# Performance work log

Hardware: AMD Instinct MI355X
Metric: run time of the kernel (lower is better)

## Reference

```python
import jax, jax.numpy as jnp
import numpy as np
import math

B, CIN, COUT, K = 32, 256, 256, 3
STYLE_DIM, SP = 512, 64  # spatial_dim == output H == output W
EPS = 1e-6


def setup_inputs() -> dict:
    key = jax.random.key(0)
    ks = jax.random.split(key, 5)
    return {
        "x": jax.random.normal(ks[0], (B, CIN, SP, SP), jnp.float32),
        "style_in": jax.random.normal(ks[1], (B, STYLE_DIM), jnp.float32),
        "weight": jax.random.normal(ks[2], (1, COUT, CIN, K, K), jnp.float32),
        "mod_w": jax.random.normal(ks[3], (CIN, STYLE_DIM // 2), jnp.float32),
        "mod_b": jnp.ones((CIN,), jnp.float32),           # bias_init=1
        "sp_w": jax.random.normal(ks[4], (SP * SP, STYLE_DIM // 2), jnp.float32),
        "sp_b": jnp.ones((SP * SP,), jnp.float32),        # bias_init=1
    }


def reference(x, style_in, weight, mod_w, mod_b, sp_w, sp_b):
    lin_scale = 1.0 / math.sqrt(STYLE_DIM // 2)   # EqualLinear scale
    conv_scale = 1.0 / math.sqrt(CIN * K * K)     # fan_in scale

    style_chan, style_spatial = jnp.split(style_in, 2, axis=1)

    # channel modulation: EqualLinear -> [B, CIN]
    style = style_chan @ (mod_w * lin_scale).T + mod_b

    # per-sample modulated weight [B, COUT, CIN, K, K]
    w = conv_scale * weight * style[:, None, :, None, None]
    demod = jax.lax.rsqrt(jnp.sum(w * w, axis=(2, 3, 4)) + EPS)  # [B, COUT]
    w = w * demod[:, :, None, None, None]

    # grouped conv2d with groups = batch ('same' padding, stride 1)
    x_g = x.reshape(1, B * CIN, SP, SP)
    w_g = w.reshape(B * COUT, CIN, K, K)
    out = jax.lax.conv_general_dilated(
        x_g, w_g, window_strides=(1, 1),
        padding=[(K // 2, K // 2), (K // 2, K // 2)],
        dimension_numbers=("NCHW", "OIHW", "NCHW"),
        feature_group_count=B,
    ).reshape(B, COUT, SP, SP)

    # spatial modulation (demod_spatial == 2): multiply by demodulated map
    sp = (style_spatial @ (sp_w * lin_scale).T + sp_b).reshape(B, 1, SP, SP)
    demod_sp = jnp.sqrt(SP * SP / jnp.sum(sp * sp, axis=(2, 3)) + EPS)  # [B, 1]
    out = out * (sp * demod_sp[:, :, None, None])
    return out
```

## Files before the change

### kernel.cpp

```cpp
#include <hip/hip_runtime.h>
#include <math.h>

typedef short short8 __attribute__((ext_vector_type(8)));
typedef float f32x4 __attribute__((ext_vector_type(4)));

#define BB 32
#define CIN 256
#define COUT 256
#define SPD 64
#define SPP 4096
#define SDIM 256

constexpr float LIN_SCALE  = 0.0625f;
constexpr float CONV_SCALE = 0.020833333333333332f;
constexpr float EPS = 1e-6f;

#define WSB_STYLE   0ULL
#define WSB_DEMOD   32768ULL
#define WSB_WSQ     65536ULL
#define WSB_SP      327680ULL
#define WSB_DSP     851968ULL
#define WSB_ZERO    852096ULL
#define WSB_WT2     860160ULL
#define WSB_SSQP    2039808ULL
#define WSB_XST     2097152ULL
#define WS_NEED     (WSB_XST + 67108864ULL)

__device__ inline unsigned short f2bf(float f) {
    unsigned u = __builtin_bit_cast(unsigned, f);
    u = (u + 0x7fffu + ((u >> 16) & 1u)) >> 16;
    return (unsigned short)u;
}

__device__ inline void dma16(const void* g, void* l) {
    __builtin_amdgcn_global_load_lds(
        (const __attribute__((address_space(1))) unsigned int*)g,
        (__attribute__((address_space(3))) unsigned int*)l, 16, 0, 0);
}

__global__ __launch_bounds__(256) void k_prepA(
    const float* __restrict__ weight,
    const float* __restrict__ style_in,
    const float* __restrict__ sp_w,
    const float* __restrict__ sp_b,
    const float* __restrict__ mod_w,
    const float* __restrict__ mod_b,
    float* __restrict__ wsq,
    unsigned short* __restrict__ wt4,
    float* __restrict__ sp,
    float* __restrict__ ssq_part,
    float* __restrict__ style,
    unsigned* __restrict__ zero)
{
    __shared__ float s_in[32][257];
    __shared__ float sred[256];
    int bid = blockIdx.x, t = threadIdx.x;

    if (bid < 256) {
        int p0 = bid * 16;
        for (int idx = t; idx < 8192; idx += 256) {
            int b = idx >> 8, k = idx & 255;
            s_in[b][k] = style_in[b * 512 + 256 + k];
        }
        __syncthreads();
        int b = t & 31, pl = t >> 5;
        float ss = 0.f;
#pragma unroll
        for (int half = 0; half < 2; half++) {
            int p = p0 + half * 8 + pl;
            const float* wr = sp_w + (size_t)p * 256;
            float a = 0.f;
            for (int k = 0; k < 256; k++) a += s_in[b][k] * wr[k];
            float v = a * LIN_SCALE + sp_b[p];
            sp[b * SPP + p] = v;
            ss += v * v;
        }
        sred[t] = ss;
        __syncthreads();
        if (t < 32) {
            float s = 0.f;
#pragma unroll
            for (int r = 0; r < 8; r++) s += sred[r * 32 + t];
            ssq_part[bid * 32 + t] = s;
        }
    } else if (bid < 2560) {
        int idx = (bid - 256) * 256 + t;
        int e    = idx & 7;
        int r1   = idx >> 3;
        int lane = r1 & 63;
        int r2   = r1 >> 6;
        int cog  = r2 & 15;
        int r3   = r2 >> 4;
        int tap  = r3 % 9;
        int kc   = r3 / 9;
        int co = cog * 16 + (lane & 15);
        int ci = kc * 32 + (lane >> 4) * 8 + e;
        wt4[idx] = f2bf(weight[(co * 256 + ci) * 9 + tap]);
    } else if (bid < 2816) {
        int co = bid - 2560, ci = t;
        if (co == 0) zero[ci] = 0u;
        const float* wp = weight + (co * CIN + ci) * 9;
        float s = 0.f;
#pragma unroll
        for (int q = 0; q < 9; q++) { float v = wp[q]; s += v * v; }
        wsq[co * CIN + ci] = s;
    } else {
        int b = bid - 2816;
        float* s_lin = &s_in[0][0];
        s_lin[t] = style_in[b * 512 + t];
        __syncthreads();
        int kq = t & 3, rr = t >> 2;
#pragma unroll
        for (int c = 0; c < 4; c++) {
            int ci = c * 64 + rr;
            const float4* wrow = (const float4*)(mod_w + (size_t)ci * 256 + kq * 64);
            float a = 0.f;
#pragma unroll
            for (int j = 0; j < 16; j++) {
                float4 wv = wrow[j];
                int kb = kq * 64 + j * 4;
                a += s_lin[kb] * wv.x + s_lin[kb + 1] * wv.y + s_lin[kb + 2] * wv.z + s_lin[kb + 3] * wv.w;
            }
            a += __shfl_xor(a, 1); a += __shfl_xor(a, 2);
            if (kq == 0) style[b * 256 + ci] = a * LIN_SCALE + mod_b[ci];
        }
    }
}

__global__ __launch_bounds__(256) void k_xt2(
    const float* __restrict__ x,
    const float* __restrict__ style,
    const float* __restrict__ wsq,
    const float* __restrict__ ssq_part,
    unsigned short* __restrict__ xst,
    float* __restrict__ demod,
    float* __restrict__ dsp)
{
    __shared__ union {
        unsigned short tileb[64][74];
        float s2[CIN];
    } sh;
    int bid = blockIdx.x, t = threadIdx.x;

    if (bid >= 2048) {
        if (bid == 2080) {
            if (t < 32) {
                float s = 0.f;
                for (int i = 0; i < 256; i++) s += ssq_part[i * 32 + t];
                dsp[t] = sqrtf((float)SPP / s + EPS);
            }
            return;
        }
        int b = bid - 2048;
        float st = style[b * 256 + t];
        sh.s2[t] = st * st;
        __syncthreads();
        int kq = t & 3, rr = t >> 2;
#pragma unroll
        for (int c = 0; c < 4; c++) {
            int co = c * 64 + rr;
            const float4* wrow = (const float4*)(wsq + (size_t)co * 256 + kq * 64);
            float a = 0.f;
#pragma unroll
            for (int j = 0; j < 16; j++) {
                float4 wv = wrow[j];
                int kb = kq * 64 + j * 4;
                a += sh.s2[kb] * wv.x + sh.s2[kb + 1] * wv.y + sh.s2[kb + 2] * wv.z + sh.s2[kb + 3] * wv.w;
            }
            a += __shfl_xor(a, 1); a += __shfl_xor(a, 2);
            if (kq == 0) demod[b * 256 + co] = rsqrtf(CONV_SCALE * CONV_SCALE * a + EPS);
        }
        return;
    }

    int b  = (bid & 7) * 4 + ((bid >> 3) & 3);
    int p0 = (bid >> 5) * 64;
    int w = t >> 6, lane = t & 63;
    int pq = lane & 15, cg = lane >> 4;
    int lo2 = t & 15;

    for (int cc = 0; cc < 4; cc++) {
#pragma unroll
        for (int j = 0; j < 4; j++) {
            int ci_l = w * 16 + j * 4 + cg;
            int ci = cc * 64 + ci_l;
            float st = style[b * 256 + ci];
            float4 v = *(const float4*)(x + ((size_t)(b * 256 + ci)) * SPP + p0 + pq * 4);
            sh.tileb[pq * 4 + 0][ci_l] = f2bf(v.x * st);
            sh.tileb[pq * 4 + 1][ci_l] = f2bf(v.y * st);
            sh.tileb[pq * 4 + 2][ci_l] = f2bf(v.z * st);
            sh.tileb[pq * 4 + 3][ci_l] = f2bf(v.w * st);
        }
        __syncthreads();
#pragma unroll
        for (int it = 0; it < 4; it++) {
            int r = it * 16 + (t >> 4);
            unsigned pk0 = (unsigned)sh.tileb[r][lo2 * 4]
                         | ((unsigned)sh.tileb[r][lo2 * 4 + 1] << 16);
            unsigned pk1 = (unsigned)sh.tileb[r][lo2 * 4 + 2]
                         | ((unsigned)sh.tileb[r][lo2 * 4 + 3] << 16);
            uint2 pv = make_uint2(pk0, pk1);
            *(uint2*)((unsigned*)xst + ((size_t)(b * SPP + p0 + r)) * 128 + cc * 32 + lo2 * 2) = pv;
        }
        __syncthreads();
    }
}

__global__ __launch_bounds__(256, 2) void k_conv_mfma(
    const unsigned short* __restrict__ xst,
    const unsigned short* __restrict__ wt4,
    const float* __restrict__ demod,
    const float* __restrict__ sp,
    const float* __restrict__ dsp,
    const unsigned short* __restrict__ zeropad,
    float* __restrict__ out)
{
    __shared__ union {
        char stage[2][25344];
        float ep[4][2176];
    } lds;
    __shared__ float demod_l[128];

    int bid = blockIdx.x;
    int xcd  = bid & 7;
    int b_lo = (bid >> 3) & 3;
    int coh  = (bid >> 5) & 1;
    int rq   = bid >> 6;
    int b  = xcd * 4 + b_lo;
    int h0 = rq * 4;
    int t = threadIdx.x;
    int w = t >> 6, lane = t & 63;
    int cpair = w & 1, rpair = w >> 1;
    int cog0 = coh * 8 + cpair * 4;
    int lcol = lane & 15, kg = lane >> 4;

    if (t < 128) demod_l[t] = demod[b * 256 + coh * 128 + t];

    const unsigned short* xb = xst + (size_t)b * SPP * 256;

    const unsigned short* sbase[7];
#pragma unroll
    for (int it = 0; it < 7; it++) {
        int idx16 = t + it * 256;
        const unsigned short* s = zeropad;
        if (idx16 < 1584) {
            int slot = idx16 >> 2, j = idx16 & 3;
            int row = slot / 66, col = slot - row * 66;
            int g = j ^ ((slot >> 1) & 3);
            int gh = h0 + row - 1, gw = col - 1;
            if ((unsigned)gh < 64u && (unsigned)gw < 64u)
                s = xb + ((size_t)(gh * 64 + gw)) * 256 + g * 8;
        }
        sbase[it] = s;
    }

#define STAGE_DMA(BUF, KC) { _Pragma("unroll") \
    for (int it = 0; it < 6; it++) \
        dma16(sbase[it] + (KC) * 32, &lds.stage[BUF][0] + (t + it * 256) * 16); \
    if (t < 48) dma16(sbase[6] + (KC) * 32, &lds.stage[BUF][0] + (t + 1536) * 16); }

    STAGE_DMA(0, 0);

    f32x4 acc[4][8];
#pragma unroll
    for (int m = 0; m < 4; m++)
#pragma unroll
        for (int n = 0; n < 8; n++) acc[m][n] = (f32x4){0.f, 0.f, 0.f, 0.f};

    asm volatile("s_waitcnt vmcnt(0) lgkmcnt(0)" ::: "memory");
    __builtin_amdgcn_s_barrier();

#define LOADW(a0,a1,a2,a3, TAP) { \
        const unsigned short* wp_ = wkc + (size_t)(((TAP) * 16 + cog0)) * 512 + lane * 8; \
        a0 = *(const short8*)(wp_); \
        a1 = *(const short8*)(wp_ + 512); \
        a2 = *(const short8*)(wp_ + 1024); \
        a3 = *(const short8*)(wp_ + 1536); }

#define LOADB(a0,a1,a2,a3, TAP, HALF) { \
        const int dh_ = (TAP) / 3, dw_ = (TAP) - 3 * (dh_); \
        int s0_ = (rpair * 2 + (HALF) + dh_) * 66 + dw_ + lcol; \
        int q_ = (s0_ >> 1) & 3; \
        const char* lbp_ = lb + s0_ * 64 + ((kg ^ q_) << 4); \
        a0 = *(const short8*)(lbp_); \
        a1 = *(const short8*)(lbp_ + 1024); \
        a2 = *(const short8*)(lbp_ + 2048); \
        a3 = *(const short8*)(lbp_ + 3072); }

#define BURSTN(w0_,w1_,w2_,w3_, x0_,x1_,x2_,x3_, NO) { \
        __builtin_amdgcn_s_setprio(1); \
        acc[0][NO+0] = __builtin_amdgcn_mfma_f32_16x16x32_bf16(w0_, x0_, acc[0][NO+0], 0, 0, 0); \
        acc[1][NO+0] = __builtin_amdgcn_mfma_f32_16x16x32_bf16(w1_, x0_, acc[1][NO+0], 0, 0, 0); \
        acc[2][NO+0] = __builtin_amdgcn_mfma_f32_16x16x32_bf16(w2_, x0_, acc[2][NO+0], 0, 0, 0); \
        acc[3][NO+0] = __builtin_amdgcn_mfma_f32_16x16x32_bf16(w3_, x0_, acc[3][NO+0], 0, 0, 0); \
        acc[0][NO+1] = __builtin_amdgcn_mfma_f32_16x16x32_bf16(w0_, x1_, acc[0][NO+1], 0, 0, 0); \
        acc[1][NO+1] = __builtin_amdgcn_mfma_f32_16x16x32_bf16(w1_, x1_, acc[1][NO+1], 0, 0, 0); \
        acc[2][NO+1] = __builtin_amdgcn_mfma_f32_16x16x32_bf16(w2_, x1_, acc[2][NO+1], 0, 0, 0); \
        acc[3][NO+1] = __builtin_amdgcn_mfma_f32_16x16x32_bf16(w3_, x1_, acc[3][NO+1], 0, 0, 0); \
        acc[0][NO+2] = __builtin_amdgcn_mfma_f32_16x16x32_bf16(w0_, x2_, acc[0][NO+2], 0, 0, 0); \
        acc[1][NO+2] = __builtin_amdgcn_mfma_f32_16x16x32_bf16(w1_, x2_, acc[1][NO+2], 0, 0, 0); \
        acc[2][NO+2] = __builtin_amdgcn_mfma_f32_16x16x32_bf16(w2_, x2_, acc[2][NO+2], 0, 0, 0); \
        acc[3][NO+2] = __builtin_amdgcn_mfma_f32_16x16x32_bf16(w3_, x2_, acc[3][NO+2], 0, 0, 0); \
        acc[0][NO+3] = __builtin_amdgcn_mfma_f32_16x16x32_bf16(w0_, x3_, acc[0][NO+3], 0, 0, 0); \
        acc[1][NO+3] = __builtin_amdgcn_mfma_f32_16x16x32_bf16(w1_, x3_, acc[1][NO+3], 0, 0, 0); \
        acc[2][NO+3] = __builtin_amdgcn_mfma_f32_16x16x32_bf16(w2_, x3_, acc[2][NO+3], 0, 0, 0); \
        acc[3][NO+3] = __builtin_amdgcn_mfma_f32_16x16x32_bf16(w3_, x3_, acc[3][NO+3], 0, 0, 0); \
        __builtin_amdgcn_s_setprio(0); }

    int cur = 0;
    for (int kc = 0; kc < 8; kc++) {
        const char* lb = &lds.stage[cur][0];
        const unsigned short* wkc = wt4 + (size_t)(kc * 9) * 8192;

        short8 wc0, wc1, wc2, wc3, wn0, wn1, wn2, wn3;
        short8 b00, b01, b02, b03, b0n0, b0n1, b0n2, b0n3;
        short8 b10, b11, b12, b13;
        LOADW(wc0, wc1, wc2, wc3, 0);
        LOADB(b00, b01, b02, b03, 0, 0);
        LOADW(wn0, wn1, wn2, wn3, 1);
        if (kc < 7) STAGE_DMA(cur ^ 1, kc + 1);

#pragma unroll
        for (int tap = 0; tap < 9; tap++) {
            if (tap >= 1 && tap < 8) {
                switch (tap + 1) {
                    case 2: LOADW(wn0,wn1,wn2,wn3,2); break;
                    case 3: LOADW(wn0,wn1,wn2,wn3,3); break;
                    case 4: LOADW(wn0,wn1,wn2,wn3,4); break;
                    case 5: LOADW(wn0,wn1,wn2,wn3,5); break;
                    case 6: LOADW(wn0,wn1,wn2,wn3,6); break;
                    case 7: LOADW(wn0,wn1,wn2,wn3,7); break;
                    case 8: LOADW(wn0,wn1,wn2,wn3,8); break;
                }
            }
            switch (tap) {
                case 0: LOADB(b10,b11,b12,b13,0,1); break;
                case 1: LOADB(b10,b11,b12,b13,1,1); break;
                case 2: LOADB(b10,b11,b12,b13,2,1); break;
                case 3: LOADB(b10,b11,b12,b13,3,1); break;
                case 4: LOADB(b10,b11,b12,b13,4,1); break;
                case 5: LOADB(b10,b11,b12,b13,5,1); break;
                case 6: LOADB(b10,b11,b12,b13,6,1); break;
                case 7: LOADB(b10,b11,b12,b13,7,1); break;
                case 8: LOADB(b10,b11,b12,b13,8,1); break;
            }
            BURSTN(wc0, wc1, wc2, wc3, b00, b01, b02, b03, 0);
            if (tap < 8) {
                switch (tap + 1) {
                    case 1: LOADB(b0n0,b0n1,b0n2,b0n3,1,0); break;
                    case 2: LOADB(b0n0,b0n1,b0n2,b0n3,2,0); break;
                    case 3: LOADB(b0n0,b0n1,b0n2,b0n3,3,0); break;
                    case 4: LOADB(b0n0,b0n1,b0n2,b0n3,4,0); break;
                    case 5: LOADB(b0n0,b0n1,b0n2,b0n3,5,0); break;
                    case 6: LOADB(b0n0,b0n1,b0n2,b0n3,6,0); break;
                    case 7: LOADB(b0n0,b0n1,b0n2,b0n3,7,0); break;
                    case 8: LOADB(b0n0,b0n1,b0n2,b0n3,8,0); break;
                }
            }
            BURSTN(wc0, wc1, wc2, wc3, b10, b11, b12, b13, 4);
            wc0 = wn0; wc1 = wn1; wc2 = wn2; wc3 = wn3;
            b00 = b0n0; b01 = b0n1; b02 = b0n2; b03 = b0n3;
        }

        asm volatile("s_waitcnt vmcnt(0) lgkmcnt(0)" ::: "memory");
        __builtin_amdgcn_s_barrier();
        cur ^= 1;
    }

    float dspb = dsp[b];
    float spn[2][4];
#pragma unroll
    for (int half = 0; half < 2; half++) {
        int hout = h0 + rpair * 2 + half;
#pragma unroll
        for (int nn = 0; nn < 4; nn++)
            spn[half][nn] = sp[b * SPP + hout * 64 + nn * 16 + lcol] * dspb;
    }

    float* ep = &lds.ep[w][0];
#pragma unroll
    for (int half = 0; half < 2; half++) {
        int hout = h0 + rpair * 2 + half;
#pragma unroll
        for (int ch = 0; ch < 2; ch++) {
#pragma unroll
            for (int mm = 0; mm < 2; mm++) {
#pragma unroll
                for (int r2 = 0; r2 < 4; r2++) {
                    int lr = mm * 16 + kg * 4 + r2;
                    float dm = demod_l[cpair * 64 + ch * 32 + lr] * CONV_SCALE;
#pragma unroll
                    for (int nn = 0; nn < 4; nn++)
                        ep[lr * 68 + nn * 16 + lcol] =
                            acc[ch * 2 + mm][half * 4 + nn][r2] * dm * spn[half][nn];
                }
            }
#pragma unroll
            for (int i = 0; i < 8; i++) {
                int lr = i * 4 + kg;
                f32x4 v = *(const f32x4*)(ep + lr * 68 + lcol * 4);
                int co_g = coh * 128 + cpair * 64 + ch * 32 + lr;
                *(f32x4*)&out[((size_t)(b * 256 + co_g)) * SPP + hout * 64 + lcol * 4] = v;
            }
        }
    }
}


__global__ void k_wsq(const float* __restrict__ weight, float* __restrict__ wsq,
                      unsigned* __restrict__ zero) {
    int co = blockIdx.x, ci = threadIdx.x;
    if (co == 0) zero[ci] = 0u;
    const float* wp = weight + (co * CIN + ci) * 9;
    float s = 0.f;
#pragma unroll
    for (int t = 0; t < 9; t++) { float v = wp[t]; s += v * v; }
    wsq[co * CIN + ci] = s;
}

__global__ void k_style_fb(const float* __restrict__ style_in,
                           const float* __restrict__ mod_w,
                           const float* __restrict__ mod_b,
                           const float* __restrict__ wsq,
                           float* __restrict__ style,
                           float* __restrict__ demod) {
    __shared__ float s_in[SDIM];
    __shared__ float s2[CIN];
    int b = blockIdx.x, t = threadIdx.x;
    s_in[t] = style_in[b * 512 + t];
    __syncthreads();
    const float* mw = mod_w + t * SDIM;
    float acc = 0.f;
    for (int k = 0; k < SDIM; k++) acc += s_in[k] * mw[k];
    float st = acc * LIN_SCALE + mod_b[t];
    style[b * CIN + t] = st;
    s2[t] = st * st;
    __syncthreads();
    const float* wq = wsq + t * CIN;
    float d = 0.f;
    for (int ci = 0; ci < CIN; ci++) d += wq[ci] * s2[ci];
    demod[b * COUT + t] = rsqrtf(CONV_SCALE * CONV_SCALE * d + EPS);
}

__global__ void k_spatial(const float* __restrict__ style_in,
                          const float* __restrict__ sp_w,
                          const float* __restrict__ sp_b,
                          float* __restrict__ sp,
                          float* __restrict__ dsp) {
    __shared__ float s_in[SDIM];
    __shared__ float red[256];
    int b = blockIdx.x, t = threadIdx.x;
    s_in[t] = style_in[b * 512 + 256 + t];
    __syncthreads();
    float ss = 0.f;
    for (int i = 0; i < 16; i++) {
        int p = i * 256 + t;
        const float* wr = sp_w + p * SDIM;
        float acc = 0.f;
        for (int k = 0; k < SDIM; k++) acc += s_in[k] * wr[k];
        float v = acc * LIN_SCALE + sp_b[p];
        sp[b * SPP + p] = v;
        ss += v * v;
    }
    red[t] = ss; __syncthreads();
    for (int o = 128; o > 0; o >>= 1) { if (t < o) red[t] += red[t + o]; __syncthreads(); }
    if (t == 0) dsp[b] = sqrtf((float)SPP / red[0] + EPS);
}

#define COTILE 16
#define TS 32
#define HALO 34
#define XS 36

__global__ __launch_bounds__(256) void k_conv_f32(
    const float* __restrict__ x, const float* __restrict__ weight,
    const float* __restrict__ style, const float* __restrict__ demod,
    const float* __restrict__ sp, const float* __restrict__ dsp,
    float* __restrict__ out) {
    __shared__ float xt[HALO * XS];
    __shared__ float wl[COTILE * 12];
    __shared__ float dml[COTILE];

    int bid = blockIdx.x;
    int tile = bid & 3;
    int cot = (bid >> 2) & 15;
    int b = bid >> 6;
    int h0 = (tile >> 1) * TS, w0 = (tile & 1) * TS;
    int t = threadIdx.x;
    int r = t >> 3;
    int cb = (t & 7) * 4;

    if (t < COTILE) dml[t] = demod[b * COUT + cot * COTILE + t];

    float acc[COTILE][4];
#pragma unroll
    for (int co = 0; co < COTILE; co++)
#pragma unroll
        for (int c = 0; c < 4; c++) acc[co][c] = 0.f;

    const float* xb = x + (size_t)b * CIN * SPP;
    const float* stb = style + b * CIN;

    for (int ci = 0; ci < CIN; ci++) {
        __syncthreads();
        const float* xc = xb + ci * SPP;
        for (int idx = t; idx < HALO * HALO; idx += 256) {
            int i = idx / HALO, j = idx - i * HALO;
            int h = h0 + i - 1, wv2 = w0 + j - 1;
            float v = 0.f;
            if ((unsigned)h < SPD && (unsigned)wv2 < SPD) v = xc[h * SPD + wv2];
            xt[i * XS + j] = v;
        }
        if (t < COTILE * 9) {
            int co = t / 9, tap = t - co * 9;
            float wv = weight[((cot * COTILE + co) * CIN + ci) * 9 + tap];
            wl[co * 12 + tap] = wv * (CONV_SCALE * stb[ci]) * dml[co];
        }
        __syncthreads();

        float xv[3][6];
#pragma unroll
        for (int dh = 0; dh < 3; dh++)
#pragma unroll
            for (int jj = 0; jj < 6; jj++)
                xv[dh][jj] = xt[(r + dh) * XS + cb + jj];

#pragma unroll
        for (int co = 0; co < COTILE; co++) {
            float w9[9];
#pragma unroll
            for (int q = 0; q < 9; q++) w9[q] = wl[co * 12 + q];
#pragma unroll
            for (int c = 0; c < 4; c++) {
                float a = acc[co][c];
#pragma unroll
                for (int dh = 0; dh < 3; dh++)
#pragma unroll
                    for (int dw = 0; dw < 3; dw++)
                        a += w9[dh * 3 + dw] * xv[dh][c + dw];
                acc[co][c] = a;
            }
        }
    }

    float dspb = dsp[b];
    int hh = h0 + r, ww = w0 + cb;
    const float* spb = sp + b * SPP + hh * SPD + ww;
    float m[4];
#pragma unroll
    for (int c = 0; c < 4; c++) m[c] = spb[c] * dspb;
#pragma unroll
    for (int co = 0; co < COTILE; co++) {
        float4 v = make_float4(acc[co][0] * m[0], acc[co][1] * m[1],
                               acc[co][2] * m[2], acc[co][3] * m[3]);
        *(float4*)&out[(size_t)((b * COUT + cot * COTILE + co) * SPP) + hh * SPD + ww] = v;
    }
}


extern "C" void kernel_launch(void* const* d_in, const int* in_sizes, int n_in,
                              void* d_out, int out_size, void* d_ws, size_t ws_size,
                              hipStream_t stream) {
    const float* x        = (const float*)d_in[0];
    const float* style_in = (const float*)d_in[1];
    const float* weight   = (const float*)d_in[2];
    const float* mod_w    = (const float*)d_in[3];
    const float* mod_b    = (const float*)d_in[4];
    const float* sp_w     = (const float*)d_in[5];
    const float* sp_b     = (const float*)d_in[6];
    float* out = (float*)d_out;
    char* wsb = (char*)d_ws;

    float* style = (float*)(wsb + WSB_STYLE);
    float* demod = (float*)(wsb + WSB_DEMOD);
    float* wsq   = (float*)(wsb + WSB_WSQ);
    float* sp    = (float*)(wsb + WSB_SP);
    float* dsp   = (float*)(wsb + WSB_DSP);
    float* ssqp  = (float*)(wsb + WSB_SSQP);
    unsigned short* wt4 = (unsigned short*)(wsb + WSB_WT2);
    unsigned short* xst = (unsigned short*)(wsb + WSB_XST);

    if (ws_size >= WS_NEED) {
        hipLaunchKernelGGL(k_prepA, dim3(2848), dim3(256), 0, stream,
                           weight, style_in, sp_w, sp_b, mod_w, mod_b,
                           wsq, wt4, sp, ssqp, style,
                           (unsigned*)(wsb + WSB_ZERO));
        hipLaunchKernelGGL(k_xt2, dim3(2081), dim3(256), 0, stream,
                           x, style, wsq, ssqp, xst, demod, dsp);
        hipLaunchKernelGGL(k_conv_mfma, dim3(1024), dim3(256), 0, stream,
                           xst, wt4, demod, sp, dsp,
                           (const unsigned short*)(wsb + WSB_ZERO), out);
    } else {
        hipLaunchKernelGGL(k_wsq, dim3(COUT), dim3(CIN), 0, stream,
                           weight, wsq, (unsigned*)(wsb + WSB_ZERO));
        hipLaunchKernelGGL(k_style_fb, dim3(BB), dim3(256), 0, stream,
                           style_in, mod_w, mod_b, wsq, style, demod);
        hipLaunchKernelGGL(k_spatial, dim3(BB), dim3(256), 0, stream,
                           style_in, sp_w, sp_b, sp, dsp);
        hipLaunchKernelGGL(k_conv_f32, dim3(2048), dim3(256), 0, stream,
                           x, weight, style, demod, sp, dsp, out);
    }
}
```

Before: 209.6 us.

## Switch conv MFMA tiles from 16x16x32 to 32x32x16 bf16

Replaces the 16x16x32 bf16 MFMA burst with 32x32x16 instructions. This means changing the packed weight layout in the prep kernel, the LDS B-operand addressing (32 pixel columns, k-halves), and the epilogue register-to-output mapping. Each wave issues 8 larger MFMAs per burst instead of 16 small ones. The larger tile gives more FLOPs per instruction and fewer operand reads per FLOP. The risk is different LDS bank-conflict behaviour with the swizzle and longer MFMA dependency latency.

```diff
diff --git a/kernel.cpp b/kernel.cpp
--- a/kernel.cpp
+++ b/kernel.cpp
@@ -3,6 +3,7 @@
 
 typedef short short8 __attribute__((ext_vector_type(8)));
 typedef float f32x4 __attribute__((ext_vector_type(4)));
+typedef float f32x16 __attribute__((ext_vector_type(16)));
 
 #define BB 32
 #define CIN 256
@@ -89,12 +90,13 @@
         int r1   = idx >> 3;
         int lane = r1 & 63;
         int r2   = r1 >> 6;
-        int cog  = r2 & 15;
+        int cogkh = r2 & 15;
+        int cog2 = cogkh >> 1, kh = cogkh & 1;
         int r3   = r2 >> 4;
         int tap  = r3 % 9;
         int kc   = r3 / 9;
-        int co = cog * 16 + (lane & 15);
-        int ci = kc * 32 + (lane >> 4) * 8 + e;
+        int co = cog2 * 32 + (lane & 31);
+        int ci = kc * 32 + kh * 16 + (lane >> 5) * 8 + e;
         wt4[idx] = f2bf(weight[(co * 256 + ci) * 9 + tap]);
     } else if (bid < 2816) {
         int co = bid - 2560, ci = t;
@@ -233,6 +235,7 @@
     int cpair = w & 1, rpair = w >> 1;
     int cog0 = coh * 8 + cpair * 4;
     int lcol = lane & 15, kg = lane >> 4;
+    int l31 = lane & 31, h5 = lane >> 5;
 
     if (t < 128) demod_l[t] = demod[b * 256 + coh * 128 + t];
 
@@ -261,50 +264,46 @@
 
     STAGE_DMA(0, 0);
 
-    f32x4 acc[4][8];
-#pragma unroll
-    for (int m = 0; m < 4; m++)
-#pragma unroll
-        for (int n = 0; n < 8; n++) acc[m][n] = (f32x4){0.f, 0.f, 0.f, 0.f};
+    f32x16 acc[2][4];
+#pragma unroll
+    for (int m = 0; m < 2; m++)
+#pragma unroll
+        for (int n = 0; n < 4; n++)
+#pragma unroll
+            for (int r = 0; r < 16; r++) acc[m][n][r] = 0.f;
 
     asm volatile("s_waitcnt vmcnt(0) lgkmcnt(0)" ::: "memory");
     __builtin_amdgcn_s_barrier();
 
-#define LOADW(a0,a1,a2,a3, TAP) { \
+#define LOADW(a00,a01,a10,a11, TAP) { \
         const unsigned short* wp_ = wkc + (size_t)(((TAP) * 16 + cog0)) * 512 + lane * 8; \
-        a0 = *(const short8*)(wp_); \
-        a1 = *(const short8*)(wp_ + 512); \
-        a2 = *(const short8*)(wp_ + 1024); \
-        a3 = *(const short8*)(wp_ + 1536); }
-
-#define LOADB(a0,a1,a2,a3, TAP, HALF) { \
+        a00 = *(const short8*)(wp_); \
+        a01 = *(const short8*)(wp_ + 512); \
+        a10 = *(const short8*)(wp_ + 1024); \
+        a11 = *(const short8*)(wp_ + 1536); }
+
+#define LOADB(b0,b1,b2,b3, TAP, HALF) { \
         const int dh_ = (TAP) / 3, dw_ = (TAP) - 3 * (dh_); \
-        int s0_ = (rpair * 2 + (HALF) + dh_) * 66 + dw_ + lcol; \
+        int s0_ = (rpair * 2 + (HALF) + dh_) * 66 + dw_ + l31; \
         int q_ = (s0_ >> 1) & 3; \
-        const char* lbp_ = lb + s0_ * 64 + ((kg ^ q_) << 4); \
-        a0 = *(const short8*)(lbp_); \
-        a1 = *(const short8*)(lbp_ + 1024); \
-        a2 = *(const short8*)(lbp_ + 2048); \
-        a3 = *(const short8*)(lbp_ + 3072); }
-
-#define BURSTN(w0_,w1_,w2_,w3_, x0_,x1_,x2_,x3_, NO) { \
+        const char* lbp_ = lb + s0_ * 64; \
+        int q0_ = (h5 ^ q_) << 4; \
+        int q1_ = ((2 + h5) ^ q_) << 4; \
+        b0 = *(const short8*)(lbp_ + q0_); \
+        b1 = *(const short8*)(lbp_ + q1_); \
+        b2 = *(const short8*)(lbp_ + 2048 + q0_); \
+        b3 = *(const short8*)(lbp_ + 2048 + q1_); }
+
+#define BURSTN(a00,a01,a10,a11, b0,b1,b2,b3, NO) { \
         __builtin_amdgcn_s_setprio(1); \
-        acc[0][NO+0] = __builtin_amdgcn_mfma_f32_16x16x32_bf16(w0_, x0_, acc[0][NO+0], 0, 0, 0); \
-        acc[1][NO+0] = __builtin_amdgcn_mfma_f32_16x16x32_bf16(w1_, x0_, acc[1][NO+0], 0, 0, 0); \
-        acc[2][NO+0] = __builtin_amdgcn_mfma_f32_16x16x32_bf16(w2_, x0_, acc[2][NO+0], 0, 0, 0); \
-        acc[3][NO+0] = __builtin_amdgcn_mfma_f32_16x16x32_bf16(w3_, x0_, acc[3][NO+0], 0, 0, 0); \
-        acc[0][NO+1] = __builtin_amdgcn_mfma_f32_16x16x32_bf16(w0_, x1_, acc[0][NO+1], 0, 0, 0); \
-        acc[1][NO+1] = __builtin_amdgcn_mfma_f32_16x16x32_bf16(w1_, x1_, acc[1][NO+1], 0, 0, 0); \
-        acc[2][NO+1] = __builtin_amdgcn_mfma_f32_16x16x32_bf16(w2_, x1_, acc[2][NO+1], 0, 0, 0); \
-        acc[3][NO+1] = __builtin_amdgcn_mfma_f32_16x16x32_bf16(w3_, x1_, acc[3][NO+1], 0, 0, 0); \
-        acc[0][NO+2] = __builtin_amdgcn_mfma_f32_16x16x32_bf16(w0_, x2_, acc[0][NO+2], 0, 0, 0); \
-        acc[1][NO+2] = __builtin_amdgcn_mfma_f32_16x16x32_bf16(w1_, x2_, acc[1][NO+2], 0, 0, 0); \
-        acc[2][NO+2] = __builtin_amdgcn_mfma_f32_16x16x32_bf16(w2_, x2_, acc[2][NO+2], 0, 0, 0); \
-        acc[3][NO+2] = __builtin_amdgcn_mfma_f32_16x16x32_bf16(w3_, x2_, acc[3][NO+2], 0, 0, 0); \
-        acc[0][NO+3] = __builtin_amdgcn_mfma_f32_16x16x32_bf16(w0_, x3_, acc[0][NO+3], 0, 0, 0); \
-        acc[1][NO+3] = __builtin_amdgcn_mfma_f32_16x16x32_bf16(w1_, x3_, acc[1][NO+3], 0, 0, 0); \
-        acc[2][NO+3] = __builtin_amdgcn_mfma_f32_16x16x32_bf16(w2_, x3_, acc[2][NO+3], 0, 0, 0); \
-        acc[3][NO+3] = __builtin_amdgcn_mfma_f32_16x16x32_bf16(w3_, x3_, acc[3][NO+3], 0, 0, 0); \
+        acc[0][NO]   = __builtin_amdgcn_mfma_f32_32x32x16_bf16(a00, b0, acc[0][NO],   0, 0, 0); \
+        acc[1][NO]   = __builtin_amdgcn_mfma_f32_32x32x16_bf16(a10, b0, acc[1][NO],   0, 0, 0); \
+        acc[0][NO+1] = __builtin_amdgcn_mfma_f32_32x32x16_bf16(a00, b2, acc[0][NO+1], 0, 0, 0); \
+        acc[1][NO+1] = __builtin_amdgcn_mfma_f32_32x32x16_bf16(a10, b2, acc[1][NO+1], 0, 0, 0); \
+        acc[0][NO]   = __builtin_amdgcn_mfma_f32_32x32x16_bf16(a01, b1, acc[0][NO],   0, 0, 0); \
+        acc[1][NO]   = __builtin_amdgcn_mfma_f32_32x32x16_bf16(a11, b1, acc[1][NO],   0, 0, 0); \
+        acc[0][NO+1] = __builtin_amdgcn_mfma_f32_32x32x16_bf16(a01, b3, acc[0][NO+1], 0, 0, 0); \
+        acc[1][NO+1] = __builtin_amdgcn_mfma_f32_32x32x16_bf16(a11, b3, acc[1][NO+1], 0, 0, 0); \
         __builtin_amdgcn_s_setprio(0); }
 
     int cur = 0;
@@ -312,25 +311,25 @@
         const char* lb = &lds.stage[cur][0];
         const unsigned short* wkc = wt4 + (size_t)(kc * 9) * 8192;
 
-        short8 wc0, wc1, wc2, wc3, wn0, wn1, wn2, wn3;
+        short8 wc00, wc01, wc10, wc11, wn00, wn01, wn10, wn11;
         short8 b00, b01, b02, b03, b0n0, b0n1, b0n2, b0n3;
         short8 b10, b11, b12, b13;
-        LOADW(wc0, wc1, wc2, wc3, 0);
+        LOADW(wc00, wc01, wc10, wc11, 0);
         LOADB(b00, b01, b02, b03, 0, 0);
-        LOADW(wn0, wn1, wn2, wn3, 1);
+        LOADW(wn00, wn01, wn10, wn11, 1);
         if (kc < 7) STAGE_DMA(cur ^ 1, kc + 1);
 
 #pragma unroll
         for (int tap = 0; tap < 9; tap++) {
             if (tap >= 1 && tap < 8) {
                 switch (tap + 1) {
-                    case 2: LOADW(wn0,wn1,wn2,wn3,2); break;
-                    case 3: LOADW(wn0,wn1,wn2,wn3,3); break;
-                    case 4: LOADW(wn0,wn1,wn2,wn3,4); break;
-                    case 5: LOADW(wn0,wn1,wn2,wn3,5); break;
-                    case 6: LOADW(wn0,wn1,wn2,wn3,6); break;
-                    case 7: LOADW(wn0,wn1,wn2,wn3,7); break;
-                    case 8: LOADW(wn0,wn1,wn2,wn3,8); break;
+                    case 2: LOADW(wn00,wn01,wn10,wn11,2); break;
+                    case 3: LOADW(wn00,wn01,wn10,wn11,3); break;
+                    case 4: LOADW(wn00,wn01,wn10,wn11,4); break;
+                    case 5: LOADW(wn00,wn01,wn10,wn11,5); break;
+                    case 6: LOADW(wn00,wn01,wn10,wn11,6); break;
+                    case 7: LOADW(wn00,wn01,wn10,wn11,7); break;
+                    case 8: LOADW(wn00,wn01,wn10,wn11,8); break;
                 }
             }
             switch (tap) {
@@ -344,7 +343,7 @@
                 case 7: LOADB(b10,b11,b12,b13,7,1); break;
                 case 8: LOADB(b10,b11,b12,b13,8,1); break;
             }
-            BURSTN(wc0, wc1, wc2, wc3, b00, b01, b02, b03, 0);
+            BURSTN(wc00, wc01, wc10, wc11, b00, b01, b02, b03, 0);
             if (tap < 8) {
                 switch (tap + 1) {
                     case 1: LOADB(b0n0,b0n1,b0n2,b0n3,1,0); break;
@@ -357,8 +356,8 @@
                     case 8: LOADB(b0n0,b0n1,b0n2,b0n3,8,0); break;
                 }
             }
-            BURSTN(wc0, wc1, wc2, wc3, b10, b11, b12, b13, 4);
-            wc0 = wn0; wc1 = wn1; wc2 = wn2; wc3 = wn3;
+            BURSTN(wc00, wc01, wc10, wc11, b10, b11, b12, b13, 2);
+            wc00 = wn00; wc01 = wn01; wc10 = wn10; wc11 = wn11;
             b00 = b0n0; b01 = b0n1; b02 = b0n2; b03 = b0n3;
         }
 
@@ -368,13 +367,13 @@
     }
 
     float dspb = dsp[b];
-    float spn[2][4];
+    float spn[2][2];
 #pragma unroll
     for (int half = 0; half < 2; half++) {
         int hout = h0 + rpair * 2 + half;
 #pragma unroll
-        for (int nn = 0; nn < 4; nn++)
-            spn[half][nn] = sp[b * SPP + hout * 64 + nn * 16 + lcol] * dspb;
+        for (int pf = 0; pf < 2; pf++)
+            spn[half][pf] = sp[b * SPP + hout * 64 + pf * 32 + l31] * dspb;
     }
 
     float* ep = &lds.ep[w][0];
@@ -382,24 +381,22 @@
     for (int half = 0; half < 2; half++) {
         int hout = h0 + rpair * 2 + half;
 #pragma unroll
-        for (int ch = 0; ch < 2; ch++) {
-#pragma unroll
-            for (int mm = 0; mm < 2; mm++) {
-#pragma unroll
-                for (int r2 = 0; r2 < 4; r2++) {
-                    int lr = mm * 16 + kg * 4 + r2;
-                    float dm = demod_l[cpair * 64 + ch * 32 + lr] * CONV_SCALE;
-#pragma unroll
-                    for (int nn = 0; nn < 4; nn++)
-                        ep[lr * 68 + nn * 16 + lcol] =
-                            acc[ch * 2 + mm][half * 4 + nn][r2] * dm * spn[half][nn];
+        for (int cf = 0; cf < 2; cf++) {
+#pragma unroll
+            for (int pf = 0; pf < 2; pf++) {
+#pragma unroll
+                for (int r = 0; r < 16; r++) {
+                    int co_l = (r & 3) + 8 * (r >> 2) + 4 * h5;
+                    float dm = demod_l[cpair * 64 + cf * 32 + co_l] * CONV_SCALE;
+                    ep[co_l * 68 + pf * 32 + l31] =
+                        acc[cf][half * 2 + pf][r] * dm * spn[half][pf];
                 }
             }
 #pragma unroll
             for (int i = 0; i < 8; i++) {
                 int lr = i * 4 + kg;
                 f32x4 v = *(const f32x4*)(ep + lr * 68 + lcol * 4);
-                int co_g = coh * 128 + cpair * 64 + ch * 32 + lr;
+                int co_g = coh * 128 + cpair * 64 + cf * 32 + lr;
                 *(f32x4*)&out[((size_t)(b * 256 + co_g)) * SPP + hout * 64 + lcol * 4] = v;
             }
         }
```

Result: slower. 241.0 us (+15.0%).
